# Kernel optimization log

Hardware: AMD Instinct MI355X
Metric: run time of the kernel (lower is better)

Reference implementation:

```python
import jax, jax.numpy as jnp
import numpy as np

B, S, C, H = 8, 1024, 768, 8
D = C // H  # head dim = 96
MLP = 4 * C


def setup_inputs() -> dict:
    key = jax.random.key(0)
    ks = jax.random.split(key, 12)
    sc = 0.02
    return {
        "x": jax.random.normal(ks[0], (B, S, C), jnp.float32),
        "ln1_w": jnp.ones((S, C), jnp.float32),
        "ln1_b": jnp.zeros((S, C), jnp.float32),
        "ln2_w": jnp.ones((S, C), jnp.float32),
        "ln2_b": jnp.zeros((S, C), jnp.float32),
        "qkv_w": jax.random.normal(ks[1], (C, 3 * C), jnp.float32) * sc,
        "proj_w": jax.random.normal(ks[2], (C, C), jnp.float32) * sc,
        "mlp_w1": jax.random.normal(ks[3], (C, MLP), jnp.float32) * sc,
        "mlp_b1": jnp.zeros((MLP,), jnp.float32),
        "mlp_w2": jax.random.normal(ks[4], (MLP, C), jnp.float32) * sc,
        "mlp_b2": jnp.zeros((C,), jnp.float32),
    }


def _layernorm2d(x, w, b, eps=1e-5):
    # normalizes over BOTH (seq, channel) dims, per nn.LayerNorm([length, channel])
    mu = jnp.mean(x, axis=(-2, -1), keepdims=True)
    var = jnp.mean(jnp.square(x - mu), axis=(-2, -1), keepdims=True)
    return (x - mu) * jax.lax.rsqrt(var + eps) * w + b


def _attention(x, qkv_w, proj_w):
    b, s, _ = x.shape
    qkv = (x @ qkv_w).reshape(b, s, 3, H, D)
    q, k, v = qkv[:, :, 0], qkv[:, :, 1], qkv[:, :, 2]  # [b, s, h, d]
    # NOTE: original module applies NO 1/sqrt(d) scaling
    scores = jnp.einsum("bshd,bthd->bhst", q, k)
    attn = jax.nn.softmax(scores, axis=-1)
    out = jnp.einsum("bhst,bthd->bshd", attn, v).reshape(b, s, C)
    return out @ proj_w


def reference(x, ln1_w, ln1_b, ln2_w, ln2_b, qkv_w, proj_w, mlp_w1, mlp_b1, mlp_w2, mlp_b2):
    # dropout is identity in eval mode
    h = x + _attention(_layernorm2d(x, ln1_w, ln1_b), qkv_w, proj_w)
    y = _layernorm2d(h, ln2_w, ln2_b)
    y = jax.nn.gelu(y @ mlp_w1 + mlp_b1, approximate=False)
    return h + (y @ mlp_w2 + mlp_b2)
```

## Files before the change

### kernel.cpp

```cpp
#include <hip/hip_runtime.h>
#include <hip/hip_bf16.h>

#define S_LEN 1024
#define NB 8
#define NC 768
#define NH 8
#define HD 96
#define NMLP 3072
#define SC (S_LEN*NC)
#define BS (NB*S_LEN)

typedef __attribute__((ext_vector_type(8))) unsigned short u16x8;
typedef __attribute__((ext_vector_type(4))) unsigned short u16x4;
typedef __attribute__((ext_vector_type(8))) __bf16 bf16x8;
typedef __attribute__((ext_vector_type(4))) float f32x4;

__device__ __forceinline__ unsigned short f2b(float f) {
  union { __hip_bfloat16 h; unsigned short u; } cvt;
  cvt.h = __float2bfloat16(f);
  return cvt.u;
}

__device__ __forceinline__ void gload16(const unsigned short* g, unsigned short* l) {
  __builtin_amdgcn_global_load_lds(
      (const __attribute__((address_space(1))) unsigned int*)g,
      (__attribute__((address_space(3))) unsigned int*)l, 16, 0, 0);
}

__device__ __forceinline__ float gelu_f(float v) {
  float u = v * (0.7978845608f + 0.0356774081f * v * v);
  float au = fabsf(u);
  float e = __expf(-2.0f * au);
  float th = (1.0f - e) / (1.0f + e);
  th = copysignf(th, u);
  return 0.5f * v * (1.0f + th);
}

template<int EPI>
__global__ __launch_bounds__(512, 1)
void gemm8(const unsigned short* __restrict__ A, int lda,
           const unsigned short* __restrict__ Bt, int ldb,
           void* __restrict__ Cv, int ldc, int K,
           const float* __restrict__ bias,
           const float* __restrict__ residual, int ldr)
{
  __shared__ unsigned short As[3*8192];
  __shared__ unsigned short Bs[3*16384];
  const int tid = threadIdx.x, lane = tid & 63, wid = tid >> 6;
  const int wm = wid & 1, wn = wid >> 1;
  const int r15 = lane & 15, g = lane >> 4;
  const int tm = blockIdx.x * 128, tn = blockIdx.y * 256;
  const int NT = K >> 6;

  const int srow = lane >> 3;
  const int scol = ((lane & 7) ^ srow) << 3;
  const unsigned short* Ag = A  + (size_t)(tm + wid*8 + srow)*lda + scol;
  const unsigned short* Bg = Bt + (size_t)(tn + wid*8 + srow)*ldb + scol;

  const int kx  = (r15 & 7) << 4;
  const int k0b = (g*16) ^ kx;
  const int k1b = (64 + g*16) ^ kx;
  char* AsB = (char*)As;
  char* BsB = (char*)Bs;
  const int arow = (wm*64 + r15) * 128;
  const int brow = (wn*64 + r15) * 128;

#define LDA8(m,ks) (*(const bf16x8*)(AsB + bufA + arow + (m)*2048 + ((ks) ? k1b : k0b)))
#define LDB8(n,ks) (*(const bf16x8*)(BsB + bufB + brow + (n)*2048 + ((ks) ? k1b : k0b)))
#define STGA(j,kk,bf) gload16(Ag + (size_t)((j)*64)*lda + (kk), As + (bf)*8192  + (j)*4096 + wid*512)
#define STGB(j,kk,bf) gload16(Bg + (size_t)((j)*64)*ldb + (kk), Bs + (bf)*16384 + (j)*4096 + wid*512)

  f32x4 acc[4][4];
  #pragma unroll
  for (int m = 0; m < 4; ++m)
    #pragma unroll
    for (int n = 0; n < 4; ++n)
      acc[m][n] = (f32x4){0.f, 0.f, 0.f, 0.f};

  STGA(0,0,0); STGA(1,0,0); STGB(0,0,0); STGB(1,0,0); STGB(2,0,0); STGB(3,0,0);
  STGA(0,64,1); STGA(1,64,1); STGB(0,64,1); STGB(1,64,1); STGB(2,64,1); STGB(3,64,1);
  asm volatile("s_waitcnt vmcnt(6)" ::: "memory");
  __builtin_amdgcn_s_barrier();

  int buf = 0, nbuf = 2;
  for (int t = 0; t < NT; ++t) {
    const int kk = (t + 2) << 6;
    const bool pre = (t + 2) < NT;
    const int bufA = buf * 16384;
    const int bufB = buf * 32768;
    bf16x8 a0[2][2], a1[2][2], b0[2][2], b1[2][2];

    if (pre) { STGA(0,kk,nbuf); STGA(1,kk,nbuf); }
    #pragma unroll
    for (int m = 0; m < 2; ++m) { a0[m][0] = LDA8(m,0); a0[m][1] = LDA8(m,1); }
    #pragma unroll
    for (int n = 0; n < 2; ++n) { b0[n][0] = LDB8(n,0); b0[n][1] = LDB8(n,1); }
    __builtin_amdgcn_s_setprio(1);
    #pragma unroll
    for (int m = 0; m < 2; ++m)
      #pragma unroll
      for (int n = 0; n < 2; ++n) {
        acc[m][n] = __builtin_amdgcn_mfma_f32_16x16x32_bf16(a0[m][0], b0[n][0], acc[m][n], 0,0,0);
        acc[m][n] = __builtin_amdgcn_mfma_f32_16x16x32_bf16(a0[m][1], b0[n][1], acc[m][n], 0,0,0);
      }
    __builtin_amdgcn_s_setprio(0);

    if (pre) { STGB(0,kk,nbuf); STGB(1,kk,nbuf); }
    #pragma unroll
    for (int n = 0; n < 2; ++n) { b1[n][0] = LDB8(n+2,0); b1[n][1] = LDB8(n+2,1); }
    __builtin_amdgcn_s_setprio(1);
    #pragma unroll
    for (int m = 0; m < 2; ++m)
      #pragma unroll
      for (int n = 0; n < 2; ++n) {
        acc[m][n+2] = __builtin_amdgcn_mfma_f32_16x16x32_bf16(a0[m][0], b1[n][0], acc[m][n+2], 0,0,0);
        acc[m][n+2] = __builtin_amdgcn_mfma_f32_16x16x32_bf16(a0[m][1], b1[n][1], acc[m][n+2], 0,0,0);
      }
    __builtin_amdgcn_s_setprio(0);

    if (pre) { STGB(2,kk,nbuf); STGB(3,kk,nbuf); }
    #pragma unroll
    for (int m = 0; m < 2; ++m) { a1[m][0] = LDA8(m+2,0); a1[m][1] = LDA8(m+2,1); }
    __builtin_amdgcn_s_setprio(1);
    #pragma unroll
    for (int m = 0; m < 2; ++m)
      #pragma unroll
      for (int n = 0; n < 2; ++n) {
        acc[m+2][n+2] = __builtin_amdgcn_mfma_f32_16x16x32_bf16(a1[m][0], b1[n][0], acc[m+2][n+2], 0,0,0);
        acc[m+2][n+2] = __builtin_amdgcn_mfma_f32_16x16x32_bf16(a1[m][1], b1[n][1], acc[m+2][n+2], 0,0,0);
      }
    __builtin_amdgcn_s_setprio(0);

    __builtin_amdgcn_s_setprio(1);
    #pragma unroll
    for (int m = 0; m < 2; ++m)
      #pragma unroll
      for (int n = 0; n < 2; ++n) {
        acc[m+2][n] = __builtin_amdgcn_mfma_f32_16x16x32_bf16(a1[m][0], b0[n][0], acc[m+2][n], 0,0,0);
        acc[m+2][n] = __builtin_amdgcn_mfma_f32_16x16x32_bf16(a1[m][1], b0[n][1], acc[m+2][n], 0,0,0);
      }
    __builtin_amdgcn_s_setprio(0);

    if (pre) asm volatile("s_waitcnt vmcnt(6)" ::: "memory");
    else     asm volatile("s_waitcnt vmcnt(0)" ::: "memory");
    __builtin_amdgcn_s_barrier();
    buf  = (buf  == 2) ? 0 : buf  + 1;
    nbuf = (nbuf == 2) ? 0 : nbuf + 1;
  }
#undef LDA8
#undef LDB8
#undef STGA
#undef STGB

  unsigned short* Cu = (unsigned short*)Cv;
  float* Cf = (float*)Cv;
  #pragma unroll
  for (int m = 0; m < 4; ++m) {
    #pragma unroll
    for (int n = 0; n < 4; ++n) {
      const int col = tn + wn*64 + n*16 + r15;
      #pragma unroll
      for (int r = 0; r < 4; ++r) {
        const int row = tm + wm*64 + m*16 + g*4 + r;
        float v = acc[m][n][r];
        if (EPI == 2 || EPI == 4) v += bias[col];
        if (EPI == 3 || EPI == 4) v += residual[(size_t)row*ldr + col];
        if (EPI == 2) v = gelu_f(v);
        if (EPI == 0 || EPI == 2) Cu[(size_t)row*ldc + col] = f2b(v);
        else                      Cf[(size_t)row*ldc + col] = v;
      }
    }
  }
}

__global__ __launch_bounds__(256, 2)
void flash_attn(const unsigned short* __restrict__ qkv,
                const unsigned short* __restrict__ vt,
                unsigned short* __restrict__ outb)
{
  __shared__ unsigned short Ks[128*96];
  __shared__ unsigned short Vs[96*128];
  __shared__ unsigned short Ps[128*128];
  const int tid = threadIdx.x, lane = tid & 63, wq = tid >> 6;
  const int r15 = lane & 15, g = lane >> 4;
  const int bh = blockIdx.y, b = bh >> 3, h = bh & 7;
  const int q0 = blockIdx.x * 128;
  const int swz = (r15 & 7) << 4;
  char* PsB = (char*)Ps;
  char* VsB = (char*)Vs;

  bf16x8 qf[2][3];
  {
    const unsigned short* qb = qkv + ((size_t)b*S_LEN + q0 + wq*32 + r15)*2304 + h*HD + g*8;
    #pragma unroll
    for (int n = 0; n < 2; ++n)
      #pragma unroll
      for (int kc = 0; kc < 3; ++kc)
        qf[n][kc] = *(const bf16x8*)(qb + (size_t)n*16*2304 + kc*32);
  }

  int krow[6], kcol[6], vrow[6], vcol[6];
  #pragma unroll
  for (int i = 0; i < 6; ++i) {
    const int c = (wq*6 + i)*64 + lane;
    krow[i] = c / 12;
    kcol[i] = (c % 12) * 8;
    const int L = c * 16;
    const int row = L >> 8, cb = L & 255;
    vrow[i] = row;
    vcol[i] = (cb ^ ((row & 7) << 4)) >> 1;
  }
  const unsigned short* kbase = qkv + (size_t)b*S_LEN*2304 + NC + h*HD;
  const unsigned short* vbase = vt + (size_t)bh*HD*S_LEN;

  f32x4 oacc[6][2];
  #pragma unroll
  for (int m = 0; m < 6; ++m) {
    oacc[m][0] = (f32x4){0.f,0.f,0.f,0.f};
    oacc[m][1] = (f32x4){0.f,0.f,0.f,0.f};
  }
  float mrun[2] = {-INFINITY, -INFINITY};
  float lrun[2] = {0.f, 0.f};

  for (int kt = 0; kt < 8; ++kt) {
    const unsigned short* ksrc = kbase + (size_t)kt*128*2304;
    const unsigned short* vsrc = vbase + kt*128;
    #pragma unroll
    for (int i = 0; i < 6; ++i) {
      gload16(ksrc + (size_t)krow[i]*2304 + kcol[i], Ks + (wq*6 + i)*512);
      gload16(vsrc + vrow[i]*1024 + vcol[i],         Vs + (wq*6 + i)*512);
    }
    __syncthreads();

    f32x4 sacc[8][2];
    #pragma unroll
    for (int m = 0; m < 8; ++m) {
      sacc[m][0] = (f32x4){0.f,0.f,0.f,0.f};
      sacc[m][1] = (f32x4){0.f,0.f,0.f,0.f};
    }
    __builtin_amdgcn_s_setprio(1);
    #pragma unroll
    for (int kc = 0; kc < 3; ++kc)
      #pragma unroll
      for (int m = 0; m < 8; ++m) {
        bf16x8 kf = *(const bf16x8*)(Ks + (m*16 + r15)*96 + kc*32 + g*8);
        sacc[m][0] = __builtin_amdgcn_mfma_f32_16x16x32_bf16(kf, qf[0][kc], sacc[m][0], 0,0,0);
        sacc[m][1] = __builtin_amdgcn_mfma_f32_16x16x32_bf16(kf, qf[1][kc], sacc[m][1], 0,0,0);
      }
    __builtin_amdgcn_s_setprio(0);

    #pragma unroll
    for (int n = 0; n < 2; ++n) {
      float pm = -INFINITY;
      #pragma unroll
      for (int m = 0; m < 8; ++m)
        #pragma unroll
        for (int r = 0; r < 4; ++r) pm = fmaxf(pm, sacc[m][n][r]);
      pm = fmaxf(pm, __shfl_xor(pm, 16));
      pm = fmaxf(pm, __shfl_xor(pm, 32));
      const float newm = fmaxf(mrun[n], pm);
      const float scale = __expf(mrun[n] - newm);
      mrun[n] = newm;
      const int qloc = wq*32 + n*16 + r15;
      float s = 0.f;
      #pragma unroll
      for (int m = 0; m < 8; ++m) {
        float e0 = __expf(sacc[m][n][0] - newm);
        float e1 = __expf(sacc[m][n][1] - newm);
        float e2 = __expf(sacc[m][n][2] - newm);
        float e3 = __expf(sacc[m][n][3] - newm);
        s += (e0 + e1) + (e2 + e3);
        u16x4 pk = { f2b(e0), f2b(e1), f2b(e2), f2b(e3) };
        *(u16x4*)(PsB + ((qloc*256 + m*32 + g*8) ^ swz)) = pk;
      }
      s += __shfl_xor(s, 16);
      s += __shfl_xor(s, 32);
      lrun[n] = lrun[n]*scale + s;
      #pragma unroll
      for (int m = 0; m < 6; ++m) oacc[m][n] *= scale;
    }

    #pragma unroll
    for (int kc = 0; kc < 4; ++kc) {
      bf16x8 pf0 = *(const bf16x8*)(PsB + (((wq*32      + r15)*256 + kc*64 + g*16) ^ swz));
      bf16x8 pf1 = *(const bf16x8*)(PsB + (((wq*32 + 16 + r15)*256 + kc*64 + g*16) ^ swz));
      __builtin_amdgcn_s_setprio(1);
      #pragma unroll
      for (int m = 0; m < 6; ++m) {
        bf16x8 vf = *(const bf16x8*)(VsB + (((m*16 + r15)*256 + kc*64 + g*16) ^ swz));
        oacc[m][0] = __builtin_amdgcn_mfma_f32_16x16x32_bf16(vf, pf0, oacc[m][0], 0,0,0);
        oacc[m][1] = __builtin_amdgcn_mfma_f32_16x16x32_bf16(vf, pf1, oacc[m][1], 0,0,0);
      }
      __builtin_amdgcn_s_setprio(0);
    }
    __syncthreads();
  }

  #pragma unroll
  for (int n = 0; n < 2; ++n) {
    const float inv = 1.0f / lrun[n];
    unsigned short* orow = outb + ((size_t)b*S_LEN + q0 + wq*32 + n*16 + r15)*NC + h*HD;
    #pragma unroll
    for (int m = 0; m < 6; ++m) {
      u16x4 pk = { f2b(oacc[m][n][0]*inv), f2b(oacc[m][n][1]*inv),
                   f2b(oacc[m][n][2]*inv), f2b(oacc[m][n][3]*inv) };
      *(u16x4*)(orow + m*16 + g*4) = pk;
    }
  }
}

__global__ void transpose_cast(const float* __restrict__ W, unsigned short* __restrict__ Wt,
                               int K, int N)
{
  __shared__ float tile[32][33];
  const int tx = threadIdx.x & 31, ty = threadIdx.x >> 5;
  const int n0 = blockIdx.x * 32, k0 = blockIdx.y * 32;
  #pragma unroll
  for (int i = 0; i < 32; i += 8)
    tile[ty + i][tx] = W[(size_t)(k0 + ty + i)*N + n0 + tx];
  __syncthreads();
  #pragma unroll
  for (int i = 0; i < 32; i += 8)
    Wt[(size_t)(n0 + ty + i)*K + k0 + tx] = f2b(tile[tx][ty + i]);
}

__global__ void transpose_v(const unsigned short* __restrict__ qkv, unsigned short* __restrict__ vt)
{
  __shared__ unsigned short tile[32][33];
  const int bh = blockIdx.z, b = bh >> 3, h = bh & 7;
  const unsigned short* v = qkv + (size_t)b*S_LEN*3*NC + 2*NC + h*HD;
  unsigned short* o = vt + (size_t)bh*HD*S_LEN;
  const int s0 = blockIdx.x * 32, d0 = blockIdx.y * 32;
  const int tx = threadIdx.x & 31, ty = threadIdx.x >> 5;
  #pragma unroll
  for (int i = 0; i < 32; i += 8)
    tile[ty + i][tx] = v[(size_t)(s0 + ty + i)*(3*NC) + d0 + tx];
  __syncthreads();
  #pragma unroll
  for (int i = 0; i < 32; i += 8)
    o[(size_t)(d0 + ty + i)*S_LEN + s0 + tx] = tile[tx][ty + i];
}

__global__ void ln_part(const float* __restrict__ X, float* __restrict__ part)
{
  const int b = blockIdx.x / 96, blk = blockIdx.x % 96;
  const float4* xb = (const float4*)(X + (size_t)b*SC);
  float s = 0.f, s2 = 0.f;
  #pragma unroll
  for (int i = 0; i < 8; ++i) {
    float4 v = xb[blk*2048 + i*256 + threadIdx.x];
    s  += v.x + v.y + v.z + v.w;
    s2 += v.x*v.x + v.y*v.y + v.z*v.z + v.w*v.w;
  }
  #pragma unroll
  for (int o = 32; o; o >>= 1) { s += __shfl_down(s, o); s2 += __shfl_down(s2, o); }
  __shared__ float r1[4], r2[4];
  const int w = threadIdx.x >> 6;
  if ((threadIdx.x & 63) == 0) { r1[w] = s; r2[w] = s2; }
  __syncthreads();
  if (threadIdx.x == 0) {
    part[(b*96 + blk)*2]     = r1[0] + r1[1] + r1[2] + r1[3];
    part[(b*96 + blk)*2 + 1] = r2[0] + r2[1] + r2[2] + r2[3];
  }
}

__global__ void ln_fin(const float* __restrict__ part, float* __restrict__ stats)
{
  const int b = blockIdx.x;
  float s = 0.f, s2 = 0.f;
  for (int i = threadIdx.x; i < 96; i += 64) {
    s  += part[(b*96 + i)*2];
    s2 += part[(b*96 + i)*2 + 1];
  }
  #pragma unroll
  for (int o = 32; o; o >>= 1) { s += __shfl_down(s, o); s2 += __shfl_down(s2, o); }
  if (threadIdx.x == 0) {
    const float inv = 1.0f / (float)SC;
    const float mu = s * inv;
    const float var = s2 * inv - mu*mu;
    stats[b*2] = mu;
    stats[b*2 + 1] = rsqrtf(var + 1e-5f);
  }
}

__global__ void ln_apply(const float* __restrict__ X, const float* __restrict__ W,
                         const float* __restrict__ Bv, const float* __restrict__ stats,
                         unsigned short* __restrict__ out)
{
  const size_t i = ((size_t)blockIdx.x*256 + threadIdx.x) * 8;
  const int b = (int)(i / SC);
  const size_t r = i % SC;
  const float mu = stats[b*2], rs = stats[b*2 + 1];
  float4 x0 = *(const float4*)(X + i),  x1 = *(const float4*)(X + i + 4);
  float4 w0 = *(const float4*)(W + r),  w1 = *(const float4*)(W + r + 4);
  float4 b0 = *(const float4*)(Bv + r), b1 = *(const float4*)(Bv + r + 4);
  u16x8 o;
  o[0] = f2b((x0.x - mu)*rs*w0.x + b0.x);
  o[1] = f2b((x0.y - mu)*rs*w0.y + b0.y);
  o[2] = f2b((x0.z - mu)*rs*w0.z + b0.z);
  o[3] = f2b((x0.w - mu)*rs*w0.w + b0.w);
  o[4] = f2b((x1.x - mu)*rs*w1.x + b1.x);
  o[5] = f2b((x1.y - mu)*rs*w1.y + b1.y);
  o[6] = f2b((x1.z - mu)*rs*w1.z + b1.z);
  o[7] = f2b((x1.w - mu)*rs*w1.w + b1.w);
  *(u16x8*)(out + i) = o;
}

extern "C" void kernel_launch(void* const* d_in, const int* in_sizes, int n_in,
                              void* d_out, int out_size, void* d_ws, size_t ws_size,
                              hipStream_t stream) {
  const float* x      = (const float*)d_in[0];
  const float* ln1_w  = (const float*)d_in[1];
  const float* ln1_b  = (const float*)d_in[2];
  const float* ln2_w  = (const float*)d_in[3];
  const float* ln2_b  = (const float*)d_in[4];
  const float* qkv_w  = (const float*)d_in[5];
  const float* proj_w = (const float*)d_in[6];
  const float* mlp_w1 = (const float*)d_in[7];
  const float* mlp_b1 = (const float*)d_in[8];
  const float* mlp_w2 = (const float*)d_in[9];
  const float* mlp_b2 = (const float*)d_in[10];
  float* out = (float*)d_out;

  char* ws = (char*)d_ws;
  size_t off = 0;
  auto alloc = [&](size_t b) { size_t o = off; off += (b + 255) & ~(size_t)255; return o; };
  unsigned short* wqkvT  = (unsigned short*)(ws + alloc((size_t)3*NC*NC*2));
  unsigned short* wprojT = (unsigned short*)(ws + alloc((size_t)NC*NC*2));
  unsigned short* w1T    = (unsigned short*)(ws + alloc((size_t)NMLP*NC*2));
  unsigned short* w2T    = (unsigned short*)(ws + alloc((size_t)NC*NMLP*2));
  unsigned short* lnbf   = (unsigned short*)(ws + alloc((size_t)BS*NC*2));
  const size_t qkvOff    = alloc((size_t)BS*3*NC*2);
  unsigned short* qkvbf  = (unsigned short*)(ws + qkvOff);
  unsigned short* vt     = (unsigned short*)(ws + alloc((size_t)NB*NH*HD*S_LEN*2));
  unsigned short* ybf    = (unsigned short*)(ws + qkvOff);
  float* hbuf            = (float*)(ws + alloc((size_t)BS*NC*4));
  float* part            = (float*)(ws + alloc((size_t)NB*96*2*4));
  float* stats           = (float*)(ws + alloc((size_t)NB*2*4));
  (void)ws_size; (void)in_sizes; (void)n_in; (void)out_size;

  const dim3 blk(256);
  const dim3 blk512(512);

  transpose_cast<<<dim3(3*NC/32, NC/32),   blk, 0, stream>>>(qkv_w,  wqkvT,  NC, 3*NC);
  transpose_cast<<<dim3(NC/32, NC/32),     blk, 0, stream>>>(proj_w, wprojT, NC, NC);
  transpose_cast<<<dim3(NMLP/32, NC/32),   blk, 0, stream>>>(mlp_w1, w1T,    NC, NMLP);
  transpose_cast<<<dim3(NC/32, NMLP/32),   blk, 0, stream>>>(mlp_w2, w2T,    NMLP, NC);

  ln_part<<<dim3(NB*96), blk, 0, stream>>>(x, part);
  ln_fin<<<dim3(NB), dim3(64), 0, stream>>>(part, stats);
  ln_apply<<<dim3(BS*NC/2048), blk, 0, stream>>>(x, ln1_w, ln1_b, stats, lnbf);

  gemm8<0><<<dim3(BS/128, 3*NC/256), blk512, 0, stream>>>(
      lnbf, NC, wqkvT, NC, qkvbf, 3*NC, NC, nullptr, nullptr, 0);

  transpose_v<<<dim3(S_LEN/32, HD/32, NB*NH), blk, 0, stream>>>(qkvbf, vt);

  flash_attn<<<dim3(S_LEN/128, NB*NH), blk, 0, stream>>>(qkvbf, vt, lnbf);

  gemm8<3><<<dim3(BS/128, NC/256), blk512, 0, stream>>>(
      lnbf, NC, wprojT, NC, hbuf, NC, NC, nullptr, x, NC);

  ln_part<<<dim3(NB*96), blk, 0, stream>>>(hbuf, part);
  ln_fin<<<dim3(NB), dim3(64), 0, stream>>>(part, stats);
  ln_apply<<<dim3(BS*NC/2048), blk, 0, stream>>>(hbuf, ln2_w, ln2_b, stats, lnbf);

  gemm8<2><<<dim3(BS/128, NMLP/256), blk512, 0, stream>>>(
      lnbf, NC, w1T, NC, ybf, NMLP, NC, mlp_b1, nullptr, 0);

  gemm8<4><<<dim3(BS/128, NC/256), blk512, 0, stream>>>(
      ybf, NMLP, w2T, NMLP, out, NC, NMLP, mlp_b2, hbuf, NC);
}
```

Before: 325.0 us.

## Switch GEMM tile to 256x128 with 4x2 warp layout and two-phase pipeline

Changes the GEMM block tile from 128x256 to 256x128, with warps arranged 4 along M by 2 along N. Each warp now keeps its whole A fragment in registers and sweeps two B halves. The main loop is restructured into two phases: global-to-LDS prefetches are placed after the LDS reads, followed by extra barriers and lgkmcnt waits. The aim is better operand reuse and cleaner overlap of loads with MFMA work, at the cost of more barriers per k-step and higher register pressure.

```diff
diff --git a/kernel.cpp b/kernel.cpp
--- a/kernel.cpp
+++ b/kernel.cpp
@@ -44,18 +44,18 @@
            const float* __restrict__ bias,
            const float* __restrict__ residual, int ldr)
 {
-  __shared__ unsigned short As[3*8192];
-  __shared__ unsigned short Bs[3*16384];
+  __shared__ unsigned short As[3*16384];
+  __shared__ unsigned short Bs[3*8192];
   const int tid = threadIdx.x, lane = tid & 63, wid = tid >> 6;
-  const int wm = wid & 1, wn = wid >> 1;
+  const int wm = wid & 3, wn = wid >> 2;
   const int r15 = lane & 15, g = lane >> 4;
-  const int tm = blockIdx.x * 128, tn = blockIdx.y * 256;
+  const int tm = blockIdx.x * 256, tn = blockIdx.y * 128;
   const int NT = K >> 6;
 
   const int srow = lane >> 3;
   const int scol = ((lane & 7) ^ srow) << 3;
-  const unsigned short* Ag = A  + (size_t)(tm + wid*8 + srow)*lda + scol;
-  const unsigned short* Bg = Bt + (size_t)(tn + wid*8 + srow)*ldb + scol;
+  const unsigned short* Ag = A  + (size_t)(tm + wid*32 + srow)*lda + scol;
+  const unsigned short* Bg = Bt + (size_t)(tn + wid*16 + srow)*ldb + scol;
 
   const int kx  = (r15 & 7) << 4;
   const int k0b = (g*16) ^ kx;
@@ -67,8 +67,9 @@
 
 #define LDA8(m,ks) (*(const bf16x8*)(AsB + bufA + arow + (m)*2048 + ((ks) ? k1b : k0b)))
 #define LDB8(n,ks) (*(const bf16x8*)(BsB + bufB + brow + (n)*2048 + ((ks) ? k1b : k0b)))
-#define STGA(j,kk,bf) gload16(Ag + (size_t)((j)*64)*lda + (kk), As + (bf)*8192  + (j)*4096 + wid*512)
-#define STGB(j,kk,bf) gload16(Bg + (size_t)((j)*64)*ldb + (kk), Bs + (bf)*16384 + (j)*4096 + wid*512)
+#define STGA(i,kk,bf) gload16(Ag + (size_t)((i)*8)*lda + (kk), As + (bf)*16384 + (wid*4 + (i))*512)
+#define STGB(i,kk,bf) gload16(Bg + (size_t)((i)*8)*ldb + (kk), Bs + (bf)*8192  + (wid*2 + (i))*512)
+#define MFMA16(a8,b8,c) __builtin_amdgcn_mfma_f32_16x16x32_bf16(a8, b8, c, 0, 0, 0)
 
   f32x4 acc[4][4];
   #pragma unroll
@@ -77,8 +78,8 @@
     for (int n = 0; n < 4; ++n)
       acc[m][n] = (f32x4){0.f, 0.f, 0.f, 0.f};
 
-  STGA(0,0,0); STGA(1,0,0); STGB(0,0,0); STGB(1,0,0); STGB(2,0,0); STGB(3,0,0);
-  STGA(0,64,1); STGA(1,64,1); STGB(0,64,1); STGB(1,64,1); STGB(2,64,1); STGB(3,64,1);
+  STGA(0,0,0); STGA(1,0,0); STGA(2,0,0); STGA(3,0,0); STGB(0,0,0); STGB(1,0,0);
+  STGA(0,64,1); STGA(1,64,1); STGA(2,64,1); STGA(3,64,1); STGB(0,64,1); STGB(1,64,1);
   asm volatile("s_waitcnt vmcnt(6)" ::: "memory");
   __builtin_amdgcn_s_barrier();
 
@@ -86,61 +87,42 @@
   for (int t = 0; t < NT; ++t) {
     const int kk = (t + 2) << 6;
     const bool pre = (t + 2) < NT;
-    const int bufA = buf * 16384;
-    const int bufB = buf * 32768;
-    bf16x8 a0[2][2], a1[2][2], b0[2][2], b1[2][2];
-
-    if (pre) { STGA(0,kk,nbuf); STGA(1,kk,nbuf); }
-    #pragma unroll
-    for (int m = 0; m < 2; ++m) { a0[m][0] = LDA8(m,0); a0[m][1] = LDA8(m,1); }
+    const int bufA = buf * 32768;
+    const int bufB = buf * 16384;
+    bf16x8 a[4][2], b0[2][2], b1[2][2];
+
+    #pragma unroll
+    for (int m = 0; m < 4; ++m) { a[m][0] = LDA8(m,0); a[m][1] = LDA8(m,1); }
     #pragma unroll
     for (int n = 0; n < 2; ++n) { b0[n][0] = LDB8(n,0); b0[n][1] = LDB8(n,1); }
+    if (pre) { STGA(0,kk,nbuf); STGA(1,kk,nbuf); STGB(0,kk,nbuf); }
+    __builtin_amdgcn_s_barrier();
+    asm volatile("s_waitcnt lgkmcnt(0)" ::: "memory");
     __builtin_amdgcn_s_setprio(1);
     #pragma unroll
-    for (int m = 0; m < 2; ++m)
+    for (int m = 0; m < 4; ++m)
       #pragma unroll
       for (int n = 0; n < 2; ++n) {
-        acc[m][n] = __builtin_amdgcn_mfma_f32_16x16x32_bf16(a0[m][0], b0[n][0], acc[m][n], 0,0,0);
-        acc[m][n] = __builtin_amdgcn_mfma_f32_16x16x32_bf16(a0[m][1], b0[n][1], acc[m][n], 0,0,0);
+        acc[m][n] = MFMA16(a[m][0], b0[n][0], acc[m][n]);
+        acc[m][n] = MFMA16(a[m][1], b0[n][1], acc[m][n]);
       }
     __builtin_amdgcn_s_setprio(0);
-
-    if (pre) { STGB(0,kk,nbuf); STGB(1,kk,nbuf); }
+    __builtin_amdgcn_s_barrier();
+
     #pragma unroll
     for (int n = 0; n < 2; ++n) { b1[n][0] = LDB8(n+2,0); b1[n][1] = LDB8(n+2,1); }
+    if (pre) { STGA(2,kk,nbuf); STGA(3,kk,nbuf); STGB(1,kk,nbuf); }
+    __builtin_amdgcn_s_barrier();
+    asm volatile("s_waitcnt lgkmcnt(0)" ::: "memory");
     __builtin_amdgcn_s_setprio(1);
     #pragma unroll
-    for (int m = 0; m < 2; ++m)
+    for (int m = 0; m < 4; ++m)
       #pragma unroll
       for (int n = 0; n < 2; ++n) {
-        acc[m][n+2] = __builtin_amdgcn_mfma_f32_16x16x32_bf16(a0[m][0], b1[n][0], acc[m][n+2], 0,0,0);
-        acc[m][n+2] = __builtin_amdgcn_mfma_f32_16x16x32_bf16(a0[m][1], b1[n][1], acc[m][n+2], 0,0,0);
+        acc[m][n+2] = MFMA16(a[m][0], b1[n][0], acc[m][n+2]);
+        acc[m][n+2] = MFMA16(a[m][1], b1[n][1], acc[m][n+2]);
       }
     __builtin_amdgcn_s_setprio(0);
-
-    if (pre) { STGB(2,kk,nbuf); STGB(3,kk,nbuf); }
-    #pragma unroll
-    for (int m = 0; m < 2; ++m) { a1[m][0] = LDA8(m+2,0); a1[m][1] = LDA8(m+2,1); }
-    __builtin_amdgcn_s_setprio(1);
-    #pragma unroll
-    for (int m = 0; m < 2; ++m)
-      #pragma unroll
-      for (int n = 0; n < 2; ++n) {
-        acc[m+2][n+2] = __builtin_amdgcn_mfma_f32_16x16x32_bf16(a1[m][0], b1[n][0], acc[m+2][n+2], 0,0,0);
-        acc[m+2][n+2] = __builtin_amdgcn_mfma_f32_16x16x32_bf16(a1[m][1], b1[n][1], acc[m+2][n+2], 0,0,0);
-      }
-    __builtin_amdgcn_s_setprio(0);
-
-    __builtin_amdgcn_s_setprio(1);
-    #pragma unroll
-    for (int m = 0; m < 2; ++m)
-      #pragma unroll
-      for (int n = 0; n < 2; ++n) {
-        acc[m+2][n] = __builtin_amdgcn_mfma_f32_16x16x32_bf16(a1[m][0], b0[n][0], acc[m+2][n], 0,0,0);
-        acc[m+2][n] = __builtin_amdgcn_mfma_f32_16x16x32_bf16(a1[m][1], b0[n][1], acc[m+2][n], 0,0,0);
-      }
-    __builtin_amdgcn_s_setprio(0);
-
     if (pre) asm volatile("s_waitcnt vmcnt(6)" ::: "memory");
     else     asm volatile("s_waitcnt vmcnt(0)" ::: "memory");
     __builtin_amdgcn_s_barrier();
@@ -151,6 +133,7 @@
 #undef LDB8
 #undef STGA
 #undef STGB
+#undef MFMA16
 
   unsigned short* Cu = (unsigned short*)Cv;
   float* Cf = (float*)Cv;
@@ -451,23 +434,23 @@
   ln_fin<<<dim3(NB), dim3(64), 0, stream>>>(part, stats);
   ln_apply<<<dim3(BS*NC/2048), blk, 0, stream>>>(x, ln1_w, ln1_b, stats, lnbf);
 
-  gemm8<0><<<dim3(BS/128, 3*NC/256), blk512, 0, stream>>>(
+  gemm8<0><<<dim3(BS/256, 3*NC/128), blk512, 0, stream>>>(
       lnbf, NC, wqkvT, NC, qkvbf, 3*NC, NC, nullptr, nullptr, 0);
 
   transpose_v<<<dim3(S_LEN/32, HD/32, NB*NH), blk, 0, stream>>>(qkvbf, vt);
 
   flash_attn<<<dim3(S_LEN/128, NB*NH), blk, 0, stream>>>(qkvbf, vt, lnbf);
 
-  gemm8<3><<<dim3(BS/128, NC/256), blk512, 0, stream>>>(
+  gemm8<3><<<dim3(BS/256, NC/128), blk512, 0, stream>>>(
       lnbf, NC, wprojT, NC, hbuf, NC, NC, nullptr, x, NC);
 
   ln_part<<<dim3(NB*96), blk, 0, stream>>>(hbuf, part);
   ln_fin<<<dim3(NB), dim3(64), 0, stream>>>(part, stats);
   ln_apply<<<dim3(BS*NC/2048), blk, 0, stream>>>(hbuf, ln2_w, ln2_b, stats, lnbf);
 
-  gemm8<2><<<dim3(BS/128, NMLP/256), blk512, 0, stream>>>(
+  gemm8<2><<<dim3(BS/256, NMLP/128), blk512, 0, stream>>>(
       lnbf, NC, w1T, NC, ybf, NMLP, NC, mlp_b1, nullptr, 0);
 
-  gemm8<4><<<dim3(BS/128, NC/256), blk512, 0, stream>>>(
+  gemm8<4><<<dim3(BS/256, NC/128), blk512, 0, stream>>>(
       ybf, NMLP, w2T, NMLP, out, NC, NMLP, mlp_b2, hbuf, NC);
 }
```

After: 283.6 us, median of 2. 12.7% less time.
